# Performance work log

Measured on AMD Instinct MI355X. Metric: run time of the kernel, lower is better.

## Reference

```python
import jax, jax.numpy as jnp
import numpy as np

N_NODES = 1024
N_EDGES = 32768
FEAT = 384
HID = 64
OUT = 64


def setup_inputs() -> dict:
    key = jax.random.key(0)
    ks = jax.random.split(key, 10)
    features = jax.random.normal(ks[0], (N_NODES, FEAT), dtype=jnp.float32)
    edge_index = jax.random.randint(ks[1], (2, N_EDGES), 0, N_NODES, dtype=jnp.int64 if jax.config.jax_enable_x64 else jnp.int32)
    edge_attr = jax.random.uniform(ks[2], (N_EDGES, 1), dtype=jnp.float32)
    # Linear weights (stored as [in, out]; torch Linear does x @ W.T)
    sc = 1.0 / np.sqrt(FEAT)
    Wk = jax.random.uniform(ks[3], (FEAT, HID), dtype=jnp.float32, minval=-sc, maxval=sc)
    Wq = jax.random.uniform(ks[4], (FEAT, HID), dtype=jnp.float32, minval=-sc, maxval=sc)
    Wv = jax.random.uniform(ks[5], (FEAT, OUT), dtype=jnp.float32, minval=-sc, maxval=sc)
    # Embedding tables, init N(0, 1)
    Ek = jax.random.normal(ks[6], (2, HID), dtype=jnp.float32)
    Eq = jax.random.normal(ks[7], (2, HID), dtype=jnp.float32)
    Ev = jax.random.normal(ks[8], (2, OUT), dtype=jnp.float32)
    bias = jnp.full((1,), 0.5, dtype=jnp.float32)
    mult = jnp.full((1,), 10.0, dtype=jnp.float32)
    return {"features": features, "edge_index": edge_index, "edge_attr": edge_attr,
            "Wk": Wk, "Wq": Wq, "Wv": Wv, "Ek": Ek, "Eq": Eq, "Ev": Ev,
            "bias": bias, "mult": mult}


def _dense_adj(src, dst, vals, n, d):
    # torch_geometric.utils.to_dense_adj: scatter-add edge attrs into [N, N, d]
    return jnp.zeros((n, n, d), vals.dtype).at[src, dst].add(vals)


def reference(features, edge_index, edge_attr, Wk, Wq, Wv, Ek, Eq, Ev, bias, mult):
    N, L = features.shape
    k = features @ Wk                      # [N, H]
    q = features @ Wq                      # [N, H]
    v = features @ Wv                      # [N, O]

    # ContinuousEmbeddingIndex: sigmoid interp, weights [E, 2]
    w = jax.nn.sigmoid((edge_attr - bias) * mult)
    w = jnp.concatenate([w, 1.0 - w], axis=-1)

    src, dst = edge_index[0], edge_index[1]
    A = q @ k.T                            # [N, N]

    # key relative embeddings (original casts to int64 -> truncate toward 0)
    rk = jnp.trunc(w @ Ek)                 # [E, H]
    Rk = _dense_adj(src, dst, rk, N, Ek.shape[1])
    A = A + jnp.einsum('ih,ijh->ij', q, Rk)

    # query relative embeddings (also truncated)
    rq = jnp.trunc(w @ Eq)
    Rq = _dense_adj(src, dst, rq, N, Eq.shape[1])
    A = A + jnp.einsum('jh,ijh->ij', k, Rq)

    # term3: (q_repeat * k_repeat).sum(-1) == q @ k.T again
    A = A + q @ k.T

    A = jax.nn.softmax(A / jnp.sqrt(jnp.asarray(L, A.dtype)), axis=-1)
    # dropout is identity at inference
    M = A @ v

    # value relative embeddings (float, no truncation)
    rv = w @ Ev                            # [E, O]
    Rv = _dense_adj(src, dst, rv, N, Ev.shape[1])
    M = M + jnp.einsum('ij,ijd->id', A, Rv)
    return M
```

## Files before the change

kernel.cpp:

```cpp
#include <hip/hip_runtime.h>
#include <math.h>

#define N_NODES 1024
#define N_EDGES 32768
#define FEAT    384

__global__ __launch_bounds__(192) void k_kqv(
        const float* __restrict__ feat,
        const float* __restrict__ Wk, const float* __restrict__ Wq,
        const float* __restrict__ Wv,
        float* __restrict__ q, float* __restrict__ k, float* __restrict__ v,
        float* __restrict__ S) {
    __shared__ float fs[4][FEAT];
    const int tid = threadIdx.x;
    const int row0 = blockIdx.x * 4;
    if (blockIdx.x == 0)
        for (int i = tid; i < 2 * N_NODES; i += 192) S[i] = 0.f;
    for (int idx = tid; idx < 4 * FEAT; idx += 192)
        fs[idx / FEAT][idx % FEAT] = feat[row0 * FEAT + idx];
    __syncthreads();

    const int col = tid & 63;
    const int which = tid >> 6;
    const float* W = (which == 0) ? Wq : (which == 1 ? Wk : Wv);
    float a0 = 0.f, a1 = 0.f, a2 = 0.f, a3 = 0.f;
    for (int f = 0; f < FEAT; ++f) {
        float wv = W[f * 64 + col];
        a0 = fmaf(fs[0][f], wv, a0);
        a1 = fmaf(fs[1][f], wv, a1);
        a2 = fmaf(fs[2][f], wv, a2);
        a3 = fmaf(fs[3][f], wv, a3);
    }
    float* out = (which == 0) ? q : (which == 1 ? k : v);
    out[(row0 + 0) * 64 + col] = a0;
    out[(row0 + 1) * 64 + col] = a1;
    out[(row0 + 2) * 64 + col] = a2;
    out[(row0 + 3) * 64 + col] = a3;
}

__global__ __launch_bounds__(256) void k_qkt(
        const float* __restrict__ q, const float* __restrict__ k,
        float* __restrict__ A) {
    __shared__ float qs[64][65];
    __shared__ float kst[64][65];
    const int tid = threadIdx.x;
    const int rowbase = blockIdx.y * 64, colbase = blockIdx.x * 64;
    for (int idx = tid; idx < 4096; idx += 256) {
        int r = idx >> 6, c = idx & 63;
        qs[r][c] = q[(rowbase + r) * 64 + c];
        kst[c][r] = k[(colbase + r) * 64 + c];
    }
    __syncthreads();
    const int tx = tid & 15, ty = tid >> 4;
    float acc[4][4] = {};
    for (int kk = 0; kk < 64; ++kk) {
        float a0 = qs[ty * 4 + 0][kk], a1 = qs[ty * 4 + 1][kk];
        float a2 = qs[ty * 4 + 2][kk], a3 = qs[ty * 4 + 3][kk];
        float b0 = kst[kk][tx * 4 + 0], b1 = kst[kk][tx * 4 + 1];
        float b2 = kst[kk][tx * 4 + 2], b3 = kst[kk][tx * 4 + 3];
        acc[0][0] = fmaf(a0, b0, acc[0][0]); acc[0][1] = fmaf(a0, b1, acc[0][1]);
        acc[0][2] = fmaf(a0, b2, acc[0][2]); acc[0][3] = fmaf(a0, b3, acc[0][3]);
        acc[1][0] = fmaf(a1, b0, acc[1][0]); acc[1][1] = fmaf(a1, b1, acc[1][1]);
        acc[1][2] = fmaf(a1, b2, acc[1][2]); acc[1][3] = fmaf(a1, b3, acc[1][3]);
        acc[2][0] = fmaf(a2, b0, acc[2][0]); acc[2][1] = fmaf(a2, b1, acc[2][1]);
        acc[2][2] = fmaf(a2, b2, acc[2][2]); acc[2][3] = fmaf(a2, b3, acc[2][3]);
        acc[3][0] = fmaf(a3, b0, acc[3][0]); acc[3][1] = fmaf(a3, b1, acc[3][1]);
        acc[3][2] = fmaf(a3, b2, acc[3][2]); acc[3][3] = fmaf(a3, b3, acc[3][3]);
    }
    for (int i = 0; i < 4; ++i) {
        float4 o = make_float4(2.f * acc[i][0], 2.f * acc[i][1],
                               2.f * acc[i][2], 2.f * acc[i][3]);
        *(float4*)&A[(size_t)(rowbase + ty * 4 + i) * N_NODES + colbase + tx * 4] = o;
    }
}

__global__ __launch_bounds__(256) void k_edgeA(
        const int* __restrict__ ei, const float* __restrict__ eattr,
        const float* __restrict__ Ek, const float* __restrict__ Eq,
        const float* __restrict__ q, const float* __restrict__ k,
        const float* __restrict__ bias, const float* __restrict__ mult,
        float* __restrict__ A, float* __restrict__ wbuf) {
    const int e = (blockIdx.x * 256 + threadIdx.x) >> 6;
    const int lane = threadIdx.x & 63;
    const int src = ei[e], dst = ei[N_EDGES + e];
    const float w  = 1.0f / (1.0f + expf(-(eattr[e] - bias[0]) * mult[0]));
    const float w1 = 1.0f - w;
    const float rk = truncf(w * Ek[lane] + w1 * Ek[64 + lane]);
    const float rq = truncf(w * Eq[lane] + w1 * Eq[64 + lane]);
    float c = q[src * 64 + lane] * rk + k[dst * 64 + lane] * rq;
    #pragma unroll
    for (int off = 32; off >= 1; off >>= 1) c += __shfl_xor(c, off, 64);
    if (lane == 0) {
        atomicAdd(&A[(size_t)src * N_NODES + dst], c);
        wbuf[e] = w;
    }
}

__global__ __launch_bounds__(256) void k_softmax(float* __restrict__ A) {
    const int row = blockIdx.x, tid = threadIdx.x;
    float4* Ar = (float4*)(A + (size_t)row * N_NODES);
    float4 x = Ar[tid];
    const float inv_s = 0.05103103630798287f;
    float m = fmaxf(fmaxf(x.x, x.y), fmaxf(x.z, x.w));
    #pragma unroll
    for (int off = 32; off >= 1; off >>= 1) m = fmaxf(m, __shfl_xor(m, off, 64));
    __shared__ float redm[4], reds[4];
    const int wid = tid >> 6, lane = tid & 63;
    if (lane == 0) redm[wid] = m;
    __syncthreads();
    m = fmaxf(fmaxf(redm[0], redm[1]), fmaxf(redm[2], redm[3]));
    float e0 = expf((x.x - m) * inv_s);
    float e1 = expf((x.y - m) * inv_s);
    float e2 = expf((x.z - m) * inv_s);
    float e3 = expf((x.w - m) * inv_s);
    float s = e0 + e1 + e2 + e3;
    #pragma unroll
    for (int off = 32; off >= 1; off >>= 1) s += __shfl_xor(s, off, 64);
    if (lane == 0) reds[wid] = s;
    __syncthreads();
    s = reds[0] + reds[1] + reds[2] + reds[3];
    float rs = 1.0f / s;
    Ar[tid] = make_float4(e0 * rs, e1 * rs, e2 * rs, e3 * rs);
}

__global__ __launch_bounds__(256) void k_edgeS(
        const int* __restrict__ ei, const float* __restrict__ wbuf,
        const float* __restrict__ A, float* __restrict__ S) {
    const int e = blockIdx.x * 256 + threadIdx.x;
    const int src = ei[e], dst = ei[N_EDGES + e];
    const float w = wbuf[e];
    const float a = A[(size_t)src * N_NODES + dst];
    atomicAdd(&S[src * 2 + 0], a * w);
    atomicAdd(&S[src * 2 + 1], a * (1.0f - w));
}

__global__ __launch_bounds__(256) void k_av(
        const float* __restrict__ A, const float* __restrict__ v,
        const float* __restrict__ Ev, const float* __restrict__ S,
        float* __restrict__ M) {
    __shared__ float As[4][N_NODES];
    __shared__ float red[4][4][64];
    const int tid = threadIdx.x;
    const int row0 = blockIdx.x * 4;
    for (int idx = tid; idx < 1024; idx += 256)
        ((float4*)As)[idx] = ((const float4*)(A + (size_t)row0 * N_NODES))[idx];
    __syncthreads();

    const int wave = tid >> 6, d = tid & 63;
    const int jbase = wave * 256;
    float acc0 = 0.f, acc1 = 0.f, acc2 = 0.f, acc3 = 0.f;
    #pragma unroll 4
    for (int j0 = 0; j0 < 256; j0 += 4) {
        const int j = jbase + j0;
        float4 a0 = *(const float4*)&As[0][j];
        float4 a1 = *(const float4*)&As[1][j];
        float4 a2 = *(const float4*)&As[2][j];
        float4 a3 = *(const float4*)&As[3][j];
        float v0 = v[(j + 0) * 64 + d];
        float v1 = v[(j + 1) * 64 + d];
        float v2 = v[(j + 2) * 64 + d];
        float v3 = v[(j + 3) * 64 + d];
        acc0 = fmaf(a0.x, v0, acc0); acc0 = fmaf(a0.y, v1, acc0);
        acc0 = fmaf(a0.z, v2, acc0); acc0 = fmaf(a0.w, v3, acc0);
        acc1 = fmaf(a1.x, v0, acc1); acc1 = fmaf(a1.y, v1, acc1);
        acc1 = fmaf(a1.z, v2, acc1); acc1 = fmaf(a1.w, v3, acc1);
        acc2 = fmaf(a2.x, v0, acc2); acc2 = fmaf(a2.y, v1, acc2);
        acc2 = fmaf(a2.z, v2, acc2); acc2 = fmaf(a2.w, v3, acc2);
        acc3 = fmaf(a3.x, v0, acc3); acc3 = fmaf(a3.y, v1, acc3);
        acc3 = fmaf(a3.z, v2, acc3); acc3 = fmaf(a3.w, v3, acc3);
    }
    red[0][wave][d] = acc0;
    red[1][wave][d] = acc1;
    red[2][wave][d] = acc2;
    red[3][wave][d] = acc3;
    __syncthreads();

    const int r = tid >> 6;
    const int row = row0 + r;
    float m = red[r][0][d] + red[r][1][d] + red[r][2][d] + red[r][3][d];
    m += S[row * 2 + 0] * Ev[d] + S[row * 2 + 1] * Ev[64 + d];
    M[row * 64 + d] = m;
}

extern "C" void kernel_launch(void* const* d_in, const int* in_sizes, int n_in,
                              void* d_out, int out_size, void* d_ws, size_t ws_size,
                              hipStream_t stream) {
    (void)in_sizes; (void)n_in; (void)out_size; (void)ws_size;
    const float* feat  = (const float*)d_in[0];
    const int*   ei    = (const int*)d_in[1];
    const float* eattr = (const float*)d_in[2];
    const float* Wk    = (const float*)d_in[3];
    const float* Wq    = (const float*)d_in[4];
    const float* Wv    = (const float*)d_in[5];
    const float* Ek    = (const float*)d_in[6];
    const float* Eq    = (const float*)d_in[7];
    const float* Ev    = (const float*)d_in[8];
    const float* bias  = (const float*)d_in[9];
    const float* mult  = (const float*)d_in[10];
    float* M = (float*)d_out;

    float* wsf = (float*)d_ws;
    float* q    = wsf;
    float* k    = wsf + 65536;
    float* v    = wsf + 131072;
    float* A    = wsf + 196608;
    float* S    = wsf + 196608 + 1048576;
    float* wbuf = S + 2048;

    k_kqv<<<256, 192, 0, stream>>>(feat, Wk, Wq, Wv, q, k, v, S);
    k_qkt<<<dim3(16, 16), 256, 0, stream>>>(q, k, A);
    k_edgeA<<<8192, 256, 0, stream>>>(ei, eattr, Ek, Eq, q, k, bias, mult, A, wbuf);
    k_softmax<<<N_NODES, 256, 0, stream>>>(A);
    k_edgeS<<<128, 256, 0, stream>>>(ei, wbuf, A, S);
    k_av<<<256, 256, 0, stream>>>(A, v, Ev, S, M);
}
```

Measured before the change: 134.0 us.

## Fuse six kernels into one cooperative megakernel with grid syncs

Replaces the six separate launches (projection, QK^T, edge score, softmax, edge sum, AV) with a single cooperative kernel of 256 blocks of 512 threads, separated by grid.sync barriers. It aims to remove per-launch overhead and inter-kernel gaps. Each stage is re-partitioned for 512 threads, with fewer rows or columns per thread and the edge stage looping 16 edges per wave. In exchange it depends on all 256 blocks being co-resident and pays for five grid-wide barriers, with lower parallelism in some stages.

```diff
diff --git a/kernel.cpp b/kernel.cpp
--- a/kernel.cpp
+++ b/kernel.cpp
@@ -1,185 +1,202 @@
 #include <hip/hip_runtime.h>
+#include <hip/hip_cooperative_groups.h>
 #include <math.h>
+
+namespace cg = cooperative_groups;
 
 #define N_NODES 1024
 #define N_EDGES 32768
 #define FEAT    384
 
-__global__ __launch_bounds__(192) void k_kqv(
-        const float* __restrict__ feat,
+__global__ __launch_bounds__(512, 1) void k_mega(
+        const float* __restrict__ feat, const int* __restrict__ ei,
+        const float* __restrict__ eattr,
         const float* __restrict__ Wk, const float* __restrict__ Wq,
         const float* __restrict__ Wv,
+        const float* __restrict__ Ek, const float* __restrict__ Eq,
+        const float* __restrict__ Ev,
+        const float* __restrict__ bias, const float* __restrict__ mult,
         float* __restrict__ q, float* __restrict__ k, float* __restrict__ v,
-        float* __restrict__ S) {
-    __shared__ float fs[4][FEAT];
-    const int tid = threadIdx.x;
-    const int row0 = blockIdx.x * 4;
-    if (blockIdx.x == 0)
-        for (int i = tid; i < 2 * N_NODES; i += 192) S[i] = 0.f;
-    for (int idx = tid; idx < 4 * FEAT; idx += 192)
-        fs[idx / FEAT][idx % FEAT] = feat[row0 * FEAT + idx];
-    __syncthreads();
-
-    const int col = tid & 63;
-    const int which = tid >> 6;
-    const float* W = (which == 0) ? Wq : (which == 1 ? Wk : Wv);
-    float a0 = 0.f, a1 = 0.f, a2 = 0.f, a3 = 0.f;
-    for (int f = 0; f < FEAT; ++f) {
-        float wv = W[f * 64 + col];
-        a0 = fmaf(fs[0][f], wv, a0);
-        a1 = fmaf(fs[1][f], wv, a1);
-        a2 = fmaf(fs[2][f], wv, a2);
-        a3 = fmaf(fs[3][f], wv, a3);
-    }
-    float* out = (which == 0) ? q : (which == 1 ? k : v);
-    out[(row0 + 0) * 64 + col] = a0;
-    out[(row0 + 1) * 64 + col] = a1;
-    out[(row0 + 2) * 64 + col] = a2;
-    out[(row0 + 3) * 64 + col] = a3;
-}
-
-__global__ __launch_bounds__(256) void k_qkt(
-        const float* __restrict__ q, const float* __restrict__ k,
-        float* __restrict__ A) {
-    __shared__ float qs[64][65];
-    __shared__ float kst[64][65];
-    const int tid = threadIdx.x;
-    const int rowbase = blockIdx.y * 64, colbase = blockIdx.x * 64;
-    for (int idx = tid; idx < 4096; idx += 256) {
-        int r = idx >> 6, c = idx & 63;
-        qs[r][c] = q[(rowbase + r) * 64 + c];
-        kst[c][r] = k[(colbase + r) * 64 + c];
-    }
-    __syncthreads();
-    const int tx = tid & 15, ty = tid >> 4;
-    float acc[4][4] = {};
-    for (int kk = 0; kk < 64; ++kk) {
-        float a0 = qs[ty * 4 + 0][kk], a1 = qs[ty * 4 + 1][kk];
-        float a2 = qs[ty * 4 + 2][kk], a3 = qs[ty * 4 + 3][kk];
-        float b0 = kst[kk][tx * 4 + 0], b1 = kst[kk][tx * 4 + 1];
-        float b2 = kst[kk][tx * 4 + 2], b3 = kst[kk][tx * 4 + 3];
-        acc[0][0] = fmaf(a0, b0, acc[0][0]); acc[0][1] = fmaf(a0, b1, acc[0][1]);
-        acc[0][2] = fmaf(a0, b2, acc[0][2]); acc[0][3] = fmaf(a0, b3, acc[0][3]);
-        acc[1][0] = fmaf(a1, b0, acc[1][0]); acc[1][1] = fmaf(a1, b1, acc[1][1]);
-        acc[1][2] = fmaf(a1, b2, acc[1][2]); acc[1][3] = fmaf(a1, b3, acc[1][3]);
-        acc[2][0] = fmaf(a2, b0, acc[2][0]); acc[2][1] = fmaf(a2, b1, acc[2][1]);
-        acc[2][2] = fmaf(a2, b2, acc[2][2]); acc[2][3] = fmaf(a2, b3, acc[2][3]);
-        acc[3][0] = fmaf(a3, b0, acc[3][0]); acc[3][1] = fmaf(a3, b1, acc[3][1]);
-        acc[3][2] = fmaf(a3, b2, acc[3][2]); acc[3][3] = fmaf(a3, b3, acc[3][3]);
-    }
-    for (int i = 0; i < 4; ++i) {
-        float4 o = make_float4(2.f * acc[i][0], 2.f * acc[i][1],
-                               2.f * acc[i][2], 2.f * acc[i][3]);
-        *(float4*)&A[(size_t)(rowbase + ty * 4 + i) * N_NODES + colbase + tx * 4] = o;
-    }
-}
-
-__global__ __launch_bounds__(256) void k_edgeA(
-        const int* __restrict__ ei, const float* __restrict__ eattr,
-        const float* __restrict__ Ek, const float* __restrict__ Eq,
-        const float* __restrict__ q, const float* __restrict__ k,
-        const float* __restrict__ bias, const float* __restrict__ mult,
-        float* __restrict__ A, float* __restrict__ wbuf) {
-    const int e = (blockIdx.x * 256 + threadIdx.x) >> 6;
-    const int lane = threadIdx.x & 63;
-    const int src = ei[e], dst = ei[N_EDGES + e];
-    const float w  = 1.0f / (1.0f + expf(-(eattr[e] - bias[0]) * mult[0]));
-    const float w1 = 1.0f - w;
-    const float rk = truncf(w * Ek[lane] + w1 * Ek[64 + lane]);
-    const float rq = truncf(w * Eq[lane] + w1 * Eq[64 + lane]);
-    float c = q[src * 64 + lane] * rk + k[dst * 64 + lane] * rq;
-    #pragma unroll
-    for (int off = 32; off >= 1; off >>= 1) c += __shfl_xor(c, off, 64);
-    if (lane == 0) {
-        atomicAdd(&A[(size_t)src * N_NODES + dst], c);
-        wbuf[e] = w;
-    }
-}
-
-__global__ __launch_bounds__(256) void k_softmax(float* __restrict__ A) {
-    const int row = blockIdx.x, tid = threadIdx.x;
-    float4* Ar = (float4*)(A + (size_t)row * N_NODES);
-    float4 x = Ar[tid];
-    const float inv_s = 0.05103103630798287f;
-    float m = fmaxf(fmaxf(x.x, x.y), fmaxf(x.z, x.w));
-    #pragma unroll
-    for (int off = 32; off >= 1; off >>= 1) m = fmaxf(m, __shfl_xor(m, off, 64));
-    __shared__ float redm[4], reds[4];
-    const int wid = tid >> 6, lane = tid & 63;
-    if (lane == 0) redm[wid] = m;
-    __syncthreads();
-    m = fmaxf(fmaxf(redm[0], redm[1]), fmaxf(redm[2], redm[3]));
-    float e0 = expf((x.x - m) * inv_s);
-    float e1 = expf((x.y - m) * inv_s);
-    float e2 = expf((x.z - m) * inv_s);
-    float e3 = expf((x.w - m) * inv_s);
-    float s = e0 + e1 + e2 + e3;
-    #pragma unroll
-    for (int off = 32; off >= 1; off >>= 1) s += __shfl_xor(s, off, 64);
-    if (lane == 0) reds[wid] = s;
-    __syncthreads();
-    s = reds[0] + reds[1] + reds[2] + reds[3];
-    float rs = 1.0f / s;
-    Ar[tid] = make_float4(e0 * rs, e1 * rs, e2 * rs, e3 * rs);
-}
-
-__global__ __launch_bounds__(256) void k_edgeS(
-        const int* __restrict__ ei, const float* __restrict__ wbuf,
-        const float* __restrict__ A, float* __restrict__ S) {
-    const int e = blockIdx.x * 256 + threadIdx.x;
-    const int src = ei[e], dst = ei[N_EDGES + e];
-    const float w = wbuf[e];
-    const float a = A[(size_t)src * N_NODES + dst];
-    atomicAdd(&S[src * 2 + 0], a * w);
-    atomicAdd(&S[src * 2 + 1], a * (1.0f - w));
-}
-
-__global__ __launch_bounds__(256) void k_av(
-        const float* __restrict__ A, const float* __restrict__ v,
-        const float* __restrict__ Ev, const float* __restrict__ S,
+        float* __restrict__ A, float* __restrict__ S, float* __restrict__ wbuf,
         float* __restrict__ M) {
-    __shared__ float As[4][N_NODES];
-    __shared__ float red[4][4][64];
-    const int tid = threadIdx.x;
-    const int row0 = blockIdx.x * 4;
-    for (int idx = tid; idx < 1024; idx += 256)
-        ((float4*)As)[idx] = ((const float4*)(A + (size_t)row0 * N_NODES))[idx];
-    __syncthreads();
-
-    const int wave = tid >> 6, d = tid & 63;
-    const int jbase = wave * 256;
-    float acc0 = 0.f, acc1 = 0.f, acc2 = 0.f, acc3 = 0.f;
-    #pragma unroll 4
-    for (int j0 = 0; j0 < 256; j0 += 4) {
-        const int j = jbase + j0;
-        float4 a0 = *(const float4*)&As[0][j];
-        float4 a1 = *(const float4*)&As[1][j];
-        float4 a2 = *(const float4*)&As[2][j];
-        float4 a3 = *(const float4*)&As[3][j];
-        float v0 = v[(j + 0) * 64 + d];
-        float v1 = v[(j + 1) * 64 + d];
-        float v2 = v[(j + 2) * 64 + d];
-        float v3 = v[(j + 3) * 64 + d];
-        acc0 = fmaf(a0.x, v0, acc0); acc0 = fmaf(a0.y, v1, acc0);
-        acc0 = fmaf(a0.z, v2, acc0); acc0 = fmaf(a0.w, v3, acc0);
-        acc1 = fmaf(a1.x, v0, acc1); acc1 = fmaf(a1.y, v1, acc1);
-        acc1 = fmaf(a1.z, v2, acc1); acc1 = fmaf(a1.w, v3, acc1);
-        acc2 = fmaf(a2.x, v0, acc2); acc2 = fmaf(a2.y, v1, acc2);
-        acc2 = fmaf(a2.z, v2, acc2); acc2 = fmaf(a2.w, v3, acc2);
-        acc3 = fmaf(a3.x, v0, acc3); acc3 = fmaf(a3.y, v1, acc3);
-        acc3 = fmaf(a3.z, v2, acc3); acc3 = fmaf(a3.w, v3, acc3);
-    }
-    red[0][wave][d] = acc0;
-    red[1][wave][d] = acc1;
-    red[2][wave][d] = acc2;
-    red[3][wave][d] = acc3;
-    __syncthreads();
-
-    const int r = tid >> 6;
-    const int row = row0 + r;
-    float m = red[r][0][d] + red[r][1][d] + red[r][2][d] + red[r][3][d];
-    m += S[row * 2 + 0] * Ev[d] + S[row * 2 + 1] * Ev[64 + d];
-    M[row * 64 + d] = m;
+    cg::grid_group grid = cg::this_grid();
+    __shared__ __align__(16) float sm[8704];
+    const int tid  = threadIdx.x;
+    const int bid  = blockIdx.x;
+    const int lane = tid & 63;
+    const int wave = tid >> 6;
+
+    {
+        float* fs = sm;
+        const int row0 = bid * 4;
+        if (tid < 384)
+            ((float4*)fs)[tid] = ((const float4*)(feat + (size_t)row0 * FEAT))[tid];
+        if (bid == 0 && tid >= 384)
+            for (int i = tid - 384; i < 2 * N_NODES; i += 128) S[i] = 0.f;
+        __syncthreads();
+        if (tid < 384) {
+            const int mat = tid >> 7;
+            const int sub = tid & 127;
+            const int col = sub & 63;
+            const int rh  = sub >> 6;
+            const float* W  = (mat == 0) ? Wq : (mat == 1 ? Wk : Wv);
+            const float* f0 = fs + (rh * 2) * FEAT;
+            const float* f1 = fs + (rh * 2 + 1) * FEAT;
+            float a0 = 0.f, a1 = 0.f;
+            #pragma unroll 8
+            for (int f = 0; f < FEAT; ++f) {
+                float wv = W[f * 64 + col];
+                a0 = fmaf(f0[f], wv, a0);
+                a1 = fmaf(f1[f], wv, a1);
+            }
+            float* out = (mat == 0) ? q : (mat == 1 ? k : v);
+            out[(row0 + rh * 2 + 0) * 64 + col] = a0;
+            out[(row0 + rh * 2 + 1) * 64 + col] = a1;
+        }
+    }
+    grid.sync();
+
+    {
+        float* qs = sm;
+        float* ks = sm + 4352;
+        const int rowbase = (bid >> 4) * 64;
+        const int colbase = (bid & 15) * 64;
+        for (int idx = tid; idx < 4096; idx += 512) {
+            int r = idx >> 6, c = idx & 63;
+            qs[r * 68 + c] = q[(rowbase + r) * 64 + c];
+            ks[c * 68 + r] = k[(colbase + r) * 64 + c];
+        }
+        __syncthreads();
+        const int tx = tid & 15, ty = tid >> 4;
+        float acc[2][4] = {};
+        for (int kk = 0; kk < 64; ++kk) {
+            float a0 = qs[(ty * 2 + 0) * 68 + kk];
+            float a1 = qs[(ty * 2 + 1) * 68 + kk];
+            float4 b = *(const float4*)&ks[kk * 68 + tx * 4];
+            acc[0][0] = fmaf(a0, b.x, acc[0][0]); acc[0][1] = fmaf(a0, b.y, acc[0][1]);
+            acc[0][2] = fmaf(a0, b.z, acc[0][2]); acc[0][3] = fmaf(a0, b.w, acc[0][3]);
+            acc[1][0] = fmaf(a1, b.x, acc[1][0]); acc[1][1] = fmaf(a1, b.y, acc[1][1]);
+            acc[1][2] = fmaf(a1, b.z, acc[1][2]); acc[1][3] = fmaf(a1, b.w, acc[1][3]);
+        }
+        #pragma unroll
+        for (int i = 0; i < 2; ++i) {
+            float4 o = make_float4(2.f * acc[i][0], 2.f * acc[i][1],
+                                   2.f * acc[i][2], 2.f * acc[i][3]);
+            *(float4*)&A[(size_t)(rowbase + ty * 2 + i) * N_NODES + colbase + tx * 4] = o;
+        }
+    }
+    grid.sync();
+
+    {
+        const int gw = (bid << 3) | wave;
+        const float b0 = bias[0], mu = mult[0];
+        const float ek0 = Ek[lane], ek1 = Ek[64 + lane];
+        const float eq0 = Eq[lane], eq1 = Eq[64 + lane];
+        #pragma unroll 2
+        for (int i = 0; i < 16; ++i) {
+            const int e = gw + i * 2048;
+            const int src = ei[e], dst = ei[N_EDGES + e];
+            const float w  = 1.0f / (1.0f + expf(-(eattr[e] - b0) * mu));
+            const float rk = truncf(w * ek0 + (1.0f - w) * ek1);
+            const float rq = truncf(w * eq0 + (1.0f - w) * eq1);
+            float c = q[src * 64 + lane] * rk + k[dst * 64 + lane] * rq;
+            #pragma unroll
+            for (int off = 32; off >= 1; off >>= 1) c += __shfl_xor(c, off, 64);
+            if (lane == 0) {
+                atomicAdd(&A[(size_t)src * N_NODES + dst], c);
+                wbuf[e] = w;
+            }
+        }
+    }
+    grid.sync();
+
+    {
+        const int g   = tid >> 7;
+        const int lt  = tid & 127;
+        const int row = bid * 4 + g;
+        float4* Ar = (float4*)(A + (size_t)row * N_NODES);
+        float4 x0 = Ar[lt * 2], x1 = Ar[lt * 2 + 1];
+        const float inv_s = 0.05103103630798287f;
+        float m = fmaxf(fmaxf(fmaxf(x0.x, x0.y), fmaxf(x0.z, x0.w)),
+                        fmaxf(fmaxf(x1.x, x1.y), fmaxf(x1.z, x1.w)));
+        #pragma unroll
+        for (int off = 32; off >= 1; off >>= 1) m = fmaxf(m, __shfl_xor(m, off, 64));
+        if (lane == 0) sm[wave] = m;
+        __syncthreads();
+        m = fmaxf(sm[g * 2], sm[g * 2 + 1]);
+        float e0 = expf((x0.x - m) * inv_s), e1 = expf((x0.y - m) * inv_s);
+        float e2 = expf((x0.z - m) * inv_s), e3 = expf((x0.w - m) * inv_s);
+        float e4 = expf((x1.x - m) * inv_s), e5 = expf((x1.y - m) * inv_s);
+        float e6 = expf((x1.z - m) * inv_s), e7 = expf((x1.w - m) * inv_s);
+        float s = ((e0 + e1) + (e2 + e3)) + ((e4 + e5) + (e6 + e7));
+        #pragma unroll
+        for (int off = 32; off >= 1; off >>= 1) s += __shfl_xor(s, off, 64);
+        if (lane == 0) sm[8 + wave] = s;
+        __syncthreads();
+        s = sm[8 + g * 2] + sm[8 + g * 2 + 1];
+        const float rs = 1.0f / s;
+        Ar[lt * 2 + 0] = make_float4(e0 * rs, e1 * rs, e2 * rs, e3 * rs);
+        Ar[lt * 2 + 1] = make_float4(e4 * rs, e5 * rs, e6 * rs, e7 * rs);
+    }
+    grid.sync();
+
+    {
+        const int e = bid * 512 + tid;
+        if (e < N_EDGES) {
+            const int src = ei[e], dst = ei[N_EDGES + e];
+            const float w = wbuf[e];
+            const float a = A[(size_t)src * N_NODES + dst];
+            atomicAdd(&S[src * 2 + 0], a * w);
+            atomicAdd(&S[src * 2 + 1], a * (1.0f - w));
+        }
+    }
+    grid.sync();
+
+    {
+        float* As  = sm;
+        float* red = sm + 4096;
+        const int row0 = bid * 4;
+        for (int idx = tid; idx < 1024; idx += 512)
+            ((float4*)As)[idx] = ((const float4*)(A + (size_t)row0 * N_NODES))[idx];
+        __syncthreads();
+        const int jbase = wave * 128;
+        const int d = lane;
+        float a0 = 0.f, a1 = 0.f, a2 = 0.f, a3 = 0.f;
+        #pragma unroll 2
+        for (int j0 = 0; j0 < 128; j0 += 4) {
+            const int j = jbase + j0;
+            float4 c0 = *(const float4*)&As[0 * 1024 + j];
+            float4 c1 = *(const float4*)&As[1 * 1024 + j];
+            float4 c2 = *(const float4*)&As[2 * 1024 + j];
+            float4 c3 = *(const float4*)&As[3 * 1024 + j];
+            float v0 = v[(j + 0) * 64 + d];
+            float v1 = v[(j + 1) * 64 + d];
+            float v2 = v[(j + 2) * 64 + d];
+            float v3 = v[(j + 3) * 64 + d];
+            a0 = fmaf(c0.x, v0, a0); a0 = fmaf(c0.y, v1, a0);
+            a0 = fmaf(c0.z, v2, a0); a0 = fmaf(c0.w, v3, a0);
+            a1 = fmaf(c1.x, v0, a1); a1 = fmaf(c1.y, v1, a1);
+            a1 = fmaf(c1.z, v2, a1); a1 = fmaf(c1.w, v3, a1);
+            a2 = fmaf(c2.x, v0, a2); a2 = fmaf(c2.y, v1, a2);
+            a2 = fmaf(c2.z, v2, a2); a2 = fmaf(c2.w, v3, a2);
+            a3 = fmaf(c3.x, v0, a3); a3 = fmaf(c3.y, v1, a3);
+            a3 = fmaf(c3.z, v2, a3); a3 = fmaf(c3.w, v3, a3);
+        }
+        red[(0 * 8 + wave) * 64 + d] = a0;
+        red[(1 * 8 + wave) * 64 + d] = a1;
+        red[(2 * 8 + wave) * 64 + d] = a2;
+        red[(3 * 8 + wave) * 64 + d] = a3;
+        __syncthreads();
+        if (tid < 256) {
+            const int r = tid >> 6, dd = tid & 63;
+            float acc = 0.f;
+            #pragma unroll
+            for (int wv = 0; wv < 8; ++wv) acc += red[(r * 8 + wv) * 64 + dd];
+            const int row = row0 + r;
+            acc += S[row * 2 + 0] * Ev[dd] + S[row * 2 + 1] * Ev[64 + dd];
+            M[row * 64 + dd] = acc;
+        }
+    }
 }
 
 extern "C" void kernel_launch(void* const* d_in, const int* in_sizes, int n_in,
@@ -207,10 +224,12 @@
     float* S    = wsf + 196608 + 1048576;
     float* wbuf = S + 2048;
 
-    k_kqv<<<256, 192, 0, stream>>>(feat, Wk, Wq, Wv, q, k, v, S);
-    k_qkt<<<dim3(16, 16), 256, 0, stream>>>(q, k, A);
-    k_edgeA<<<8192, 256, 0, stream>>>(ei, eattr, Ek, Eq, q, k, bias, mult, A, wbuf);
-    k_softmax<<<N_NODES, 256, 0, stream>>>(A);
-    k_edgeS<<<128, 256, 0, stream>>>(ei, wbuf, A, S);
-    k_av<<<256, 256, 0, stream>>>(A, v, Ev, S, M);
+    void* args[] = {(void*)&feat, (void*)&ei, (void*)&eattr,
+                    (void*)&Wk, (void*)&Wq, (void*)&Wv,
+                    (void*)&Ek, (void*)&Eq, (void*)&Ev,
+                    (void*)&bias, (void*)&mult,
+                    (void*)&q, (void*)&k, (void*)&v,
+                    (void*)&A, (void*)&S, (void*)&wbuf, (void*)&M};
+    hipLaunchCooperativeKernel((const void*)k_mega, dim3(256), dim3(512),
+                               args, 0, stream);
 }
```

Measured after the change: 286.2 us. 114% more time.
